# Kernel optimization log

Hardware: AMD Instinct MI355X
Metric: run time of the kernel (lower is better)

Reference implementation:

```python
import jax, jax.numpy as jnp
import numpy as np

TOP_K = 48
NUM_RBF = 16
NUM_RBF_SC = 8
MAXREL = 32
EDGE_F = 128
EPS_D = 1e-6
LN_EPS = 1e-5


def gather_nodes(nodes, idx):
    # nodes: [B, L, C], idx: [B, L, K] -> [B, L, K, C]
    return jax.vmap(lambda n, i: n[i])(nodes, idx)


def rbf(D, count):
    # D: [..., ] -> [..., count]; mu in [2, 22], sigma = 20/count
    mu = jnp.linspace(2.0, 22.0, count)
    sigma = (22.0 - 2.0) / count
    return jnp.exp(-(((D[..., None] - mu) / sigma) ** 2))


def layer_norm(x, g, b):
    mu = jnp.mean(x, -1, keepdims=True)
    var = jnp.mean((x - mu) ** 2, -1, keepdims=True)
    return g * (x - mu) / jnp.sqrt(var + LN_EPS) + b


def setup_inputs() -> dict:
    key = jax.random.key(0)
    ks = jax.random.split(key, 8)
    B, Lr = 1, 1024
    X = jax.random.normal(ks[0], (B, Lr, 37, 3), dtype=jnp.float32)
    mask = jnp.ones((B, Lr), dtype=jnp.float32)
    atom_mask = jnp.ones((B, Lr, 37), dtype=jnp.float32)
    residue_idx = jnp.arange(B * Lr, dtype=jnp.int64 if jax.config.jax_enable_x64 else jnp.int32).reshape(B, Lr)
    dihedral_mask = jnp.ones((B, Lr), dtype=jnp.float32)
    chain_labels = jnp.zeros((B, Lr), dtype=jnp.int32)
    W_pos = jax.random.normal(ks[1], (16, 2 * MAXREL + 2), dtype=jnp.float32) * 0.1
    b_pos = jnp.zeros((16,), dtype=jnp.float32)
    W_e = jax.random.normal(ks[2], (EDGE_F, 16 + NUM_RBF * 25), dtype=jnp.float32) * 0.05
    g_e = jnp.ones((EDGE_F,), dtype=jnp.float32)
    be_e = jnp.zeros((EDGE_F,), dtype=jnp.float32)
    W_s = jax.random.normal(ks[3], (EDGE_F, NUM_RBF_SC * 32 * 5), dtype=jnp.float32) * 0.05
    g_s = jnp.ones((EDGE_F,), dtype=jnp.float32)
    b_s = jnp.zeros((EDGE_F,), dtype=jnp.float32)
    return {"X": X, "L": 1024, "mask": mask, "atom_mask": atom_mask,
            "residue_idx": residue_idx, "dihedral_mask": dihedral_mask,
            "chain_labels": chain_labels, "W_pos": W_pos, "b_pos": b_pos,
            "W_e": W_e, "g_e": g_e, "be_e": be_e, "W_s": W_s, "g_s": g_s, "b_s": b_s}


def reference(X, L, mask, atom_mask, residue_idx, dihedral_mask, chain_labels,
              W_pos, b_pos, W_e, g_e, be_e, W_s, g_s, b_s):
    # Virtual Cb from ideal geometry
    b_v = X[:, :, 1, :] - X[:, :, 0, :]
    c_v = X[:, :, 2, :] - X[:, :, 1, :]
    a_v = jnp.cross(b_v, c_v)
    Cb = -0.58273431 * a_v + 0.56802827 * b_v - 0.54067466 * c_v + X[:, :, 1, :]
    Ca = X[:, :, 1, :]
    N = X[:, :, 0, :]
    C = X[:, :, 2, :]
    O = X[:, :, 4, :]

    # _dist: masked pairwise Ca distances + top-k smallest
    mask2d = mask[:, None, :] * mask[:, :, None]  # [B, L, L]
    dX = Ca[:, :, None, :] - Ca[:, None, :, :]
    D = mask2d * jnp.sqrt(jnp.sum(dX ** 2, -1) + EPS_D)
    D_max = jnp.max(D, -1, keepdims=True)
    D_adj = D + (1.0 - mask2d) * D_max
    neg_vals, E_idx = jax.lax.top_k(-D_adj, TOP_K)
    D_neighbors = -neg_vals  # [B, L, K]

    coords = {'N': N, 'Ca': Ca, 'C': C, 'O': O, 'Cb': Cb}
    pairs = [('N','N'),('C','C'),('O','O'),('Cb','Cb'),('Ca','N'),('Ca','C'),('Ca','O'),
             ('Ca','Cb'),('N','C'),('N','O'),('N','Cb'),('Cb','C'),('Cb','O'),('O','C'),
             ('N','Ca'),('C','Ca'),('O','Ca'),('Cb','Ca'),('C','N'),('O','N'),('Cb','N'),
             ('C','Cb'),('O','Cb'),('C','O')]
    A_st = jnp.stack([coords[a] for a, _ in pairs])  # [24, B, L, 3]
    B_st = jnp.stack([coords[b] for _, b in pairs])
    B_nb = jax.vmap(gather_nodes, (0, None))(B_st, E_idx)  # [24, B, L, K, 3]
    Dp = jnp.sqrt(jnp.sum((A_st[:, :, :, None, :] - B_nb) ** 2, -1) + EPS_D)  # [24,B,L,K]
    RBF_pairs = rbf(Dp, NUM_RBF)  # [24, B, L, K, 16]
    Bt, Lr, K = E_idx.shape
    RBF_pairs = jnp.moveaxis(RBF_pairs, 0, 3).reshape(Bt, Lr, K, 24 * NUM_RBF)
    RBF_all = jnp.concatenate([rbf(D_neighbors, NUM_RBF), RBF_pairs], -1)  # [B,L,K,400]

    # Positional encodings
    ri_nb = gather_nodes(residue_idx[..., None], E_idx)[..., 0]  # [B,L,K]
    offset = residue_idx[:, :, None] - ri_nb
    ch_nb = gather_nodes(chain_labels[..., None], E_idx)[..., 0]
    E_chains = (chain_labels[:, :, None] - ch_nb == 0).astype(jnp.int32)
    d = jnp.clip(offset + MAXREL, 0, 2 * MAXREL) * E_chains + (1 - E_chains) * (2 * MAXREL + 1)
    d_onehot = jax.nn.one_hot(d, 2 * MAXREL + 2, dtype=jnp.float32)
    E_positional = d_onehot @ W_pos.T + b_pos
    E = jnp.concatenate([E_positional, RBF_all], -1)  # [B,L,K,416]

    # Sidechain RBFs on the first min(100, K) neighbors
    Ks = min(100, K)
    E_idx_sub = E_idx[:, :, :Ks]
    am_g = gather_nodes(atom_mask, E_idx_sub)  # [B,L,Ks,37]
    S = X[:, :, 5:37, :]  # [B,L,32,3]
    S_nb = gather_nodes(S.reshape(Bt, Lr, 32 * 3), E_idx_sub).reshape(Bt, Lr, Ks, 32, 3)
    anchors = jnp.stack([N, Ca, C, O, Cb], 2)  # [B,L,5,3], anchor order matches loop order
    Ds = jnp.sqrt(jnp.sum((anchors[:, :, None, :, None, :] - S_nb[:, :, :, None, :, :]) ** 2, -1) + EPS_D)
    # Ds: [B,L,Ks,5,32]; rbf_side -> [B,L,Ks,5,32,8]; masked by neighbor atom mask
    RBF_s = rbf(Ds, NUM_RBF_SC) * am_g[:, :, :, None, 5:37, None]
    E_s = RBF_s.reshape(Bt, Lr, Ks, 5 * 32 * NUM_RBF_SC)  # [B,L,Ks,1280]

    E_s = layer_norm(E_s @ W_s.T, g_s, b_s)
    E = layer_norm(E @ W_e.T, g_e, be_e)
    return (E, E_idx, E_s, E_idx_sub)
```

## Files before the change

kernel.cpp:

```cpp
#include <hip/hip_runtime.h>
#include <math.h>

#define LRES 1024
#define TOPK 48
#define NEDGE (LRES*TOPK)

typedef short short8 __attribute__((ext_vector_type(8)));
typedef float f32x4  __attribute__((ext_vector_type(4)));

#define OUT_E     0
#define OUT_EIDX  6291456
#define OUT_ES    6340608
#define OUT_EIDX2 12632064

#define WS_COORDS 0
#define WS_DNB    15360
#define WS_EIDX   64512
#define WS_WPE    113664
#define WS_WPS    146432

#define DE 1.06666667f
#define QE 0.10273976f
#define DS 1.14285714f
#define QS 0.07337053f

__constant__ int PA[24] = {0,2,3,4,1,1,1,1,0,0,0,4,4,3,0,2,3,4,2,3,4,2,3,2};
__constant__ int PB[24] = {0,2,3,4,0,2,3,4,2,3,4,2,3,2,1,1,1,1,0,0,0,4,4,3};

__device__ inline short f2bf(float f) {
    unsigned u = __float_as_uint(f);
    unsigned r = (u + 0x7FFFu + ((u >> 16) & 1u)) >> 16;
    return (short)r;
}

__device__ inline short8 pack8(const float* fv) {
    union { short8 s; unsigned u[4]; } r;
    #pragma unroll
    for (int i = 0; i < 4; ++i)
        r.u[i] = __builtin_amdgcn_perm(__float_as_uint(fv[2*i+1]),
                                       __float_as_uint(fv[2*i]), 0x07060302u);
    return r.s;
}

__global__ __launch_bounds__(256) void k_pre(const float* __restrict__ X,
                                             const float* __restrict__ mask,
                                             const float* __restrict__ We,
                                             const float* __restrict__ Ws,
                                             float* __restrict__ coords,
                                             short* __restrict__ WpE,
                                             short* __restrict__ WpS,
                                             float* __restrict__ Dnb,
                                             int* __restrict__ Eidx,
                                             float* __restrict__ out) {
    int blk = blockIdx.x, t = threadIdx.x;
    if (blk < 256) {
        __shared__ float sCa[LRES*3];
        __shared__ float sM[LRES];
        for (int j = t; j < LRES; j += 256) {
            sCa[j*3+0] = X[j*111 + 3];
            sCa[j*3+1] = X[j*111 + 4];
            sCa[j*3+2] = X[j*111 + 5];
            sM[j] = mask[j];
        }
        __syncthreads();
        int w = t >> 6, lane = t & 63;
        int i = blk * 4 + w;
        float cx = sCa[i*3], cy = sCa[i*3+1], cz = sCa[i*3+2];
        float mi = sM[i];
        float dv[16], m2v[16];
        float lmax = -1e30f;
        #pragma unroll
        for (int s = 0; s < 16; ++s) {
            int j = s*64 + lane;
            float dx = cx - sCa[j*3], dy = cy - sCa[j*3+1], dz = cz - sCa[j*3+2];
            float d  = __builtin_amdgcn_sqrtf(dx*dx + dy*dy + dz*dz + 1e-6f);
            float m2 = mi * sM[j];
            dv[s] = m2 * d; m2v[s] = m2;
            lmax = fmaxf(lmax, dv[s]);
        }
        #pragma unroll
        for (int off = 32; off; off >>= 1) lmax = fmaxf(lmax, __shfl_xor(lmax, off));
        unsigned long long key[16];
        #pragma unroll
        for (int s = 0; s < 16; ++s) {
            float dadj = dv[s] + (1.0f - m2v[s]) * lmax;
            key[s] = (((unsigned long long)__float_as_uint(dadj)) << 10) | (unsigned)(s*64 + lane);
        }
        unsigned long long mkey = key[0];
        #pragma unroll
        for (int s = 1; s < 16; ++s) mkey = (key[s] < mkey) ? key[s] : mkey;
        for (int it = 0; it < TOPK; ++it) {
            unsigned long long wk = mkey;
            #pragma unroll
            for (int off = 32; off; off >>= 1) {
                unsigned long long o = __shfl_xor(wk, off);
                wk = (o < wk) ? o : wk;
            }
            if (lane == 0) {
                int j = (int)(wk & 1023u);
                int id = i*TOPK + it;
                Dnb[id]  = __uint_as_float((unsigned)(wk >> 10));
                Eidx[id] = j;
                out[OUT_EIDX  + id] = (float)j;
                out[OUT_EIDX2 + id] = (float)j;
            }
            if (mkey == wk) {
                #pragma unroll
                for (int s = 0; s < 16; ++s)
                    key[s] = (key[s] == wk) ? ~0ull : key[s];
                mkey = key[0];
                #pragma unroll
                for (int s = 1; s < 16; ++s) mkey = (key[s] < mkey) ? key[s] : mkey;
            }
        }
    } else if (blk < 896) {
        int g = (blk - 256) * 256 + t;
        if (g < 8*16*64*8) {
            int j = g & 7, lane = (g >> 3) & 63, gg = g >> 9;
            int ks = gg & 15, nt = gg >> 4;
            int n = nt*16 + (lane & 15), k = ks*32 + (lane >> 4)*8 + j;
            WpE[g] = (k < 416) ? f2bf(We[n*416 + k]) : (short)0;
        }
        if (g < 8*40*64*8) {
            int j = g & 7, lane = (g >> 3) & 63, gg = g >> 9;
            int ks = gg % 40, nt = gg / 40;
            int n = nt*16 + (lane & 15), k = ks*32 + (lane >> 4)*8 + j;
            WpS[g] = f2bf(Ws[n*1280 + k]);
        }
    } else {
        int r = (blk - 896) * 256 + t;
        if (r >= LRES) return;
        const float* xr = X + r * 111;
        float N[3], Ca[3], C[3], O[3], bv[3], cv[3], av[3];
        #pragma unroll
        for (int d = 0; d < 3; ++d) {
            N[d]  = xr[0*3 + d];  Ca[d] = xr[1*3 + d];
            C[d]  = xr[2*3 + d];  O[d]  = xr[4*3 + d];
            bv[d] = Ca[d] - N[d]; cv[d] = C[d] - Ca[d];
        }
        av[0] = bv[1]*cv[2] - bv[2]*cv[1];
        av[1] = bv[2]*cv[0] - bv[0]*cv[2];
        av[2] = bv[0]*cv[1] - bv[1]*cv[0];
        float* o = coords + r * 15;
        #pragma unroll
        for (int d = 0; d < 3; ++d) {
            float Cb = -0.58273431f*av[d] + 0.56802827f*bv[d] - 0.54067466f*cv[d] + Ca[d];
            o[0*3+d] = N[d]; o[1*3+d] = Ca[d]; o[2*3+d] = C[d];
            o[3*3+d] = O[d]; o[4*3+d] = Cb;
        }
    }
}

__global__ __launch_bounds__(256, 3) void k_edge(const float* __restrict__ coords,
                                                 const float* __restrict__ X,
                                                 const float* __restrict__ amask,
                                                 const short* __restrict__ WpE,
                                                 const short* __restrict__ WpS,
                                                 const float* __restrict__ Dnb,
                                                 const int* __restrict__ Eidx,
                                                 const int* __restrict__ ri,
                                                 const int* __restrict__ ch,
                                                 const float* __restrict__ Wpos,
                                                 const float* __restrict__ bpos,
                                                 const float* __restrict__ ge,
                                                 const float* __restrict__ be,
                                                 const float* __restrict__ gs,
                                                 const float* __restrict__ bs,
                                                 float* __restrict__ out) {
    __shared__ float smem[9104];
    float* Ar    = smem;
    float* Br    = smem + 4224;
    float* part  = smem + 8448;
    float* part2 = smem + 8704;
    float* smu   = smem + 8960;
    float* srs   = smem + 8992;
    int*   sdpos = (int*)(smem + 9024);
    float* sA3   = smem + 9056;

    int t = threadIdx.x;
    int w = t >> 6, lane = t & 63, quad = lane >> 4, l16 = lane & 15;
    bool isS = blockIdx.x < 1536;
    int id0 = (isS ? blockIdx.x : blockIdx.x - 1536) * 32;

    f32x4 acc[2][8] = {};
    size_t outBase;
    const float *gW, *bW;

    if (isS) {
        outBase = OUT_ES; gW = gs; bW = bs;
        int i0 = id0 / TOPK;
        if (t < 45) {
            int rr = i0 + t / 15;
            if (rr > LRES-1) rr = LRES-1;
            sA3[t] = coords[rr*15 + t%15];
        }
        int s1 = 4*w + quad;
        float S[2][2][3], am[2][2];
        int bA[2];
        #pragma unroll
        for (int mt = 0; mt < 2; ++mt) {
            int id = id0 + mt*16 + l16;
            int j  = Eidx[id];
            bA[mt] = (id / TOPK - i0) * 15;
            const float* xp = X + (j*37 + 5)*3;
            const float* ap = amask + j*37 + 5;
            #pragma unroll
            for (int h = 0; h < 2; ++h) {
                int s = s1 + h*16;
                S[mt][h][0] = xp[s*3+0];
                S[mt][h][1] = xp[s*3+1];
                S[mt][h][2] = xp[s*3+2];
                am[mt][h]   = ap[s];
            }
        }
        __syncthreads();

        const short8* bp = (const short8*)WpS;
        for (int a = 0; a < 5; ++a) {
            float A[2][3];
            #pragma unroll
            for (int mt = 0; mt < 2; ++mt) {
                A[mt][0] = sA3[bA[mt] + a*3+0];
                A[mt][1] = sA3[bA[mt] + a*3+1];
                A[mt][2] = sA3[bA[mt] + a*3+2];
            }
            #pragma unroll
            for (int h = 0; h < 2; ++h) {
                int ks = a*8 + w + h*4;
                short8 afrag[2];
                #pragma unroll
                for (int mt = 0; mt < 2; ++mt) {
                    float dx = A[mt][0] - S[mt][h][0];
                    float dy = A[mt][1] - S[mt][h][1];
                    float dz = A[mt][2] - S[mt][h][2];
                    float d  = __builtin_amdgcn_sqrtf(fmaf(dz,dz,fmaf(dy,dy,fmaf(dx,dx,1e-6f))));
                    float u  = fmaf(d, 0.4f, -0.8f);
                    float e0 = __expf(-u*u) * am[mt][h];
                    float g  = __expf(fmaf(2.0f*DS, u, -(DS*DS)));
                    float fv[8];
                    fv[0] = e0;
                    #pragma unroll
                    for (int r = 1; r < 8; ++r) { e0 *= g; g *= QS; fv[r] = e0; }
                    afrag[mt] = pack8(fv);
                }
                #pragma unroll
                for (int nt = 0; nt < 8; ++nt) {
                    short8 b = bp[(nt*40 + ks)*64 + lane];
                    acc[0][nt] = __builtin_amdgcn_mfma_f32_16x16x32_bf16(afrag[0], b, acc[0][nt], 0,0,0);
                    acc[1][nt] = __builtin_amdgcn_mfma_f32_16x16x32_bf16(afrag[1], b, acc[1][nt], 0,0,0);
                }
            }
        }
    } else {
        outBase = OUT_E; gW = ge; bW = be;
        float* sdist = Ar;
        float* sposf = Ar + 900;
        float* sA    = Br;
        float* sB    = Br + 480;

        if (t < 32) {
            int id = id0 + t, i = id / TOPK, j = Eidx[id];
            int off = ri[i] - ri[j];
            sdpos[t] = (ch[i] == ch[j]) ? min(max(off + 32, 0), 64) : 65;
            sdist[t*27] = Dnb[id];
        }
        for (int it = t; it < 32*15; it += 256) {
            int e = it / 15, q = it % 15;
            int id = id0 + e, i = id / TOPK, j = Eidx[id];
            sA[e*15+q] = coords[i*15+q];
            sB[e*15+q] = coords[j*15+q];
        }
        __syncthreads();
        for (int it = t; it < 32*24; it += 256) {
            int e = it / 24, p = it % 24, a = PA[p], b = PB[p];
            float dx = sA[e*15+a*3+0] - sB[e*15+b*3+0];
            float dy = sA[e*15+a*3+1] - sB[e*15+b*3+1];
            float dz = sA[e*15+a*3+2] - sB[e*15+b*3+2];
            sdist[e*27 + 1 + p] = __builtin_amdgcn_sqrtf(dx*dx + dy*dy + dz*dz + 1e-6f);
        }
        for (int it = t; it < 32*16; it += 256) {
            int e = it >> 4, c = it & 15;
            sposf[e*17 + c] = Wpos[c*66 + sdpos[e]] + bpos[c];
        }
        __syncthreads();

        const short8* bp = (const short8*)WpE;
        float rb = (quad & 1) ? 8.0f*DE : 0.0f;
        for (int ks = w; ks < 16; ks += 4) {
            short8 afrag[2];
            #pragma unroll
            for (int mt = 0; mt < 2; ++mt) {
                int e = mt*16 + l16;
                float fv[8];
                if (ks == 0 && quad < 2) {
                    #pragma unroll
                    for (int j = 0; j < 8; ++j) fv[j] = sposf[e*17 + quad*8 + j];
                } else {
                    int p = (ks == 0) ? 0 : (2*ks - 1 + (quad >> 1));
                    float d = sdist[e*27 + p];
                    float u = fmaf(d, 0.8f, -1.6f) - rb;
                    float e0 = __expf(-u*u);
                    float g  = __expf(fmaf(2.0f*DE, u, -(DE*DE)));
                    fv[0] = e0;
                    #pragma unroll
                    for (int r = 1; r < 8; ++r) { e0 *= g; g *= QE; fv[r] = e0; }
                }
                afrag[mt] = pack8(fv);
            }
            #pragma unroll
            for (int nt = 0; nt < 8; ++nt) {
                short8 b = bp[(nt*16 + ks)*64 + lane];
                acc[0][nt] = __builtin_amdgcn_mfma_f32_16x16x32_bf16(afrag[0], b, acc[0][nt], 0,0,0);
                acc[1][nt] = __builtin_amdgcn_mfma_f32_16x16x32_bf16(afrag[1], b, acc[1][nt], 0,0,0);
            }
        }
        __syncthreads();
    }

    if (w < 2) {
        float* R = (w == 0) ? Ar : Br;
        #pragma unroll
        for (int mt = 0; mt < 2; ++mt)
        #pragma unroll
        for (int nt = 0; nt < 8; ++nt)
        #pragma unroll
        for (int r = 0; r < 4; ++r)
            R[(mt*16 + quad*4 + r)*132 + nt*16 + l16] = acc[mt][nt][r];
    }
    __syncthreads();
    if (w >= 2) {
        float* R = (w == 2) ? Ar : Br;
        #pragma unroll
        for (int mt = 0; mt < 2; ++mt)
        #pragma unroll
        for (int nt = 0; nt < 8; ++nt)
        #pragma unroll
        for (int r = 0; r < 4; ++r)
            R[(mt*16 + quad*4 + r)*132 + nt*16 + l16] += acc[mt][nt][r];
    }
    __syncthreads();
    {
        int e = t >> 3, p = t & 7;
        float s = 0.f, s2 = 0.f;
        #pragma unroll
        for (int q = 0; q < 16; ++q) {
            int f = q*8 + p;
            float x = Ar[e*132 + f] + Br[e*132 + f];
            Ar[e*132 + f] = x;
            s += x; s2 += x*x;
        }
        part[e*8+p] = s; part2[e*8+p] = s2;
    }
    __syncthreads();
    if (t < 32) {
        float s = 0.f, s2 = 0.f;
        #pragma unroll
        for (int p = 0; p < 8; ++p) { s += part[t*8+p]; s2 += part2[t*8+p]; }
        float mu = s * (1.0f/128.0f);
        float var = s2 * (1.0f/128.0f) - mu*mu;
        smu[t] = mu; srs[t] = rsqrtf(var + 1e-5f);
    }
    __syncthreads();
    for (int it = t; it < 32*32; it += 256) {
        int e = it >> 5, f = (it & 31)*4;
        float4 x = *(const float4*)&Ar[e*132 + f];
        float4 G = *(const float4*)&gW[f];
        float4 B = *(const float4*)&bW[f];
        float mu = smu[e], rs = srs[e];
        float4 r;
        r.x = G.x*(x.x - mu)*rs + B.x;
        r.y = G.y*(x.y - mu)*rs + B.y;
        r.z = G.z*(x.z - mu)*rs + B.z;
        r.w = G.w*(x.w - mu)*rs + B.w;
        *(float4*)&out[outBase + (size_t)(id0 + e)*128 + f] = r;
    }
}

extern "C" void kernel_launch(void* const* d_in, const int* in_sizes, int n_in,
                              void* d_out, int out_size, void* d_ws, size_t ws_size,
                              hipStream_t stream) {
    (void)in_sizes; (void)n_in; (void)out_size; (void)ws_size;
    const float* X     = (const float*)d_in[0];
    const float* mask  = (const float*)d_in[2];
    const float* amask = (const float*)d_in[3];
    const int*   ri    = (const int*)d_in[4];
    const int*   ch    = (const int*)d_in[6];
    const float* Wpos  = (const float*)d_in[7];
    const float* bpos  = (const float*)d_in[8];
    const float* We    = (const float*)d_in[9];
    const float* ge    = (const float*)d_in[10];
    const float* be    = (const float*)d_in[11];
    const float* Ws    = (const float*)d_in[12];
    const float* gs    = (const float*)d_in[13];
    const float* bs    = (const float*)d_in[14];

    float* out    = (float*)d_out;
    float* ws     = (float*)d_ws;
    float* coords = ws + WS_COORDS;
    float* Dnb    = ws + WS_DNB;
    int*   Eidx   = (int*)(ws + WS_EIDX);
    short* WpE    = (short*)(ws + WS_WPE);
    short* WpS    = (short*)(ws + WS_WPS);

    k_pre <<<dim3(900),  dim3(256), 0, stream>>>(X, mask, We, Ws, coords,
                                                 WpE, WpS, Dnb, Eidx, out);
    k_edge<<<dim3(3072), dim3(256), 0, stream>>>(coords, X, amask, WpE, WpS,
                                                 Dnb, Eidx, ri, ch, Wpos, bpos,
                                                 ge, be, gs, bs, out);
}
```

Measured before the change: 190.8 us.

## Split waves across N-tiles and K-halves, shrink LDS, raise occupancy

Each wave now owns half of the 128 output columns and half of the K slices, instead of all columns over a quarter of K. This halves the accumulator registers per wave and replaces the two row-major reduction buffers with one column-major buffer. Shared memory falls from about 36KB to about 21KB, and launch bounds go from 3 to 4 blocks per SM. The E path also stops after K slice 12, skipping the zero-padded slices beyond the 416 real features. In exchange, the RBF A-fragments are computed twice (once by each column-half wave), and the final layer-norm store becomes scalar, strided writes instead of float4 rows.

```diff
diff --git a/kernel.cpp b/kernel.cpp
--- a/kernel.cpp
+++ b/kernel.cpp
@@ -151,7 +151,7 @@
     }
 }
 
-__global__ __launch_bounds__(256, 3) void k_edge(const float* __restrict__ coords,
+__global__ __launch_bounds__(256, 4) void k_edge(const float* __restrict__ coords,
                                                  const float* __restrict__ X,
                                                  const float* __restrict__ amask,
                                                  const short* __restrict__ WpE,
@@ -167,22 +167,22 @@
                                                  const float* __restrict__ gs,
                                                  const float* __restrict__ bs,
                                                  float* __restrict__ out) {
-    __shared__ float smem[9104];
-    float* Ar    = smem;
-    float* Br    = smem + 4224;
-    float* part  = smem + 8448;
-    float* part2 = smem + 8704;
-    float* smu   = smem + 8960;
-    float* srs   = smem + 8992;
-    int*   sdpos = (int*)(smem + 9024);
-    float* sA3   = smem + 9056;
+    __shared__ float smem[5264];
+    float* colbuf = smem;
+    float* part   = smem + 4608;
+    float* part2  = smem + 4864;
+    float* smu    = smem + 5120;
+    float* srs    = smem + 5152;
+    int*   sdpos  = (int*)(smem + 5184);
+    float* sA3    = smem + 5216;
 
     int t = threadIdx.x;
     int w = t >> 6, lane = t & 63, quad = lane >> 4, l16 = lane & 15;
+    int tm = w & 1, kp = w >> 1;
     bool isS = blockIdx.x < 1536;
     int id0 = (isS ? blockIdx.x : blockIdx.x - 1536) * 32;
 
-    f32x4 acc[2][8] = {};
+    f32x4 acc[2][4] = {};
     size_t outBase;
     const float *gW, *bW;
 
@@ -194,8 +194,7 @@
             if (rr > LRES-1) rr = LRES-1;
             sA3[t] = coords[rr*15 + t%15];
         }
-        int s1 = 4*w + quad;
-        float S[2][2][3], am[2][2];
+        float S[2][4][3], am[2][4];
         int bA[2];
         #pragma unroll
         for (int mt = 0; mt < 2; ++mt) {
@@ -205,38 +204,38 @@
             const float* xp = X + (j*37 + 5)*3;
             const float* ap = amask + j*37 + 5;
             #pragma unroll
-            for (int h = 0; h < 2; ++h) {
-                int s = s1 + h*16;
-                S[mt][h][0] = xp[s*3+0];
-                S[mt][h][1] = xp[s*3+1];
-                S[mt][h][2] = xp[s*3+2];
-                am[mt][h]   = ap[s];
+            for (int u = 0; u < 4; ++u) {
+                int s = 4*kp + quad + 8*u;
+                S[mt][u][0] = xp[s*3+0];
+                S[mt][u][1] = xp[s*3+1];
+                S[mt][u][2] = xp[s*3+2];
+                am[mt][u]   = ap[s];
             }
         }
         __syncthreads();
 
         const short8* bp = (const short8*)WpS;
         for (int a = 0; a < 5; ++a) {
-            float A[2][3];
+            float A0[2][3];
             #pragma unroll
             for (int mt = 0; mt < 2; ++mt) {
-                A[mt][0] = sA3[bA[mt] + a*3+0];
-                A[mt][1] = sA3[bA[mt] + a*3+1];
-                A[mt][2] = sA3[bA[mt] + a*3+2];
-            }
-            #pragma unroll
-            for (int h = 0; h < 2; ++h) {
-                int ks = a*8 + w + h*4;
+                A0[mt][0] = sA3[bA[mt] + a*3+0];
+                A0[mt][1] = sA3[bA[mt] + a*3+1];
+                A0[mt][2] = sA3[bA[mt] + a*3+2];
+            }
+            #pragma unroll
+            for (int u = 0; u < 4; ++u) {
+                int ks = a*8 + kp + 2*u;
                 short8 afrag[2];
                 #pragma unroll
                 for (int mt = 0; mt < 2; ++mt) {
-                    float dx = A[mt][0] - S[mt][h][0];
-                    float dy = A[mt][1] - S[mt][h][1];
-                    float dz = A[mt][2] - S[mt][h][2];
+                    float dx = A0[mt][0] - S[mt][u][0];
+                    float dy = A0[mt][1] - S[mt][u][1];
+                    float dz = A0[mt][2] - S[mt][u][2];
                     float d  = __builtin_amdgcn_sqrtf(fmaf(dz,dz,fmaf(dy,dy,fmaf(dx,dx,1e-6f))));
-                    float u  = fmaf(d, 0.4f, -0.8f);
-                    float e0 = __expf(-u*u) * am[mt][h];
-                    float g  = __expf(fmaf(2.0f*DS, u, -(DS*DS)));
+                    float uu = fmaf(d, 0.4f, -0.8f);
+                    float e0 = __expf(-uu*uu) * am[mt][u];
+                    float g  = __expf(fmaf(2.0f*DS, uu, -(DS*DS)));
                     float fv[8];
                     fv[0] = e0;
                     #pragma unroll
@@ -244,19 +243,19 @@
                     afrag[mt] = pack8(fv);
                 }
                 #pragma unroll
-                for (int nt = 0; nt < 8; ++nt) {
-                    short8 b = bp[(nt*40 + ks)*64 + lane];
-                    acc[0][nt] = __builtin_amdgcn_mfma_f32_16x16x32_bf16(afrag[0], b, acc[0][nt], 0,0,0);
-                    acc[1][nt] = __builtin_amdgcn_mfma_f32_16x16x32_bf16(afrag[1], b, acc[1][nt], 0,0,0);
+                for (int n = 0; n < 4; ++n) {
+                    short8 b = bp[((tm*4 + n)*40 + ks)*64 + lane];
+                    acc[0][n] = __builtin_amdgcn_mfma_f32_16x16x32_bf16(afrag[0], b, acc[0][n], 0,0,0);
+                    acc[1][n] = __builtin_amdgcn_mfma_f32_16x16x32_bf16(afrag[1], b, acc[1][n], 0,0,0);
                 }
             }
         }
     } else {
         outBase = OUT_E; gW = ge; bW = be;
-        float* sdist = Ar;
-        float* sposf = Ar + 900;
-        float* sA    = Br;
-        float* sB    = Br + 480;
+        float* sdist = colbuf;
+        float* sposf = colbuf + 900;
+        float* sAc   = colbuf + 1472;
+        float* sBc   = colbuf + 1952;
 
         if (t < 32) {
             int id = id0 + t, i = id / TOPK, j = Eidx[id];
@@ -267,15 +266,15 @@
         for (int it = t; it < 32*15; it += 256) {
             int e = it / 15, q = it % 15;
             int id = id0 + e, i = id / TOPK, j = Eidx[id];
-            sA[e*15+q] = coords[i*15+q];
-            sB[e*15+q] = coords[j*15+q];
+            sAc[e*15+q] = coords[i*15+q];
+            sBc[e*15+q] = coords[j*15+q];
         }
         __syncthreads();
         for (int it = t; it < 32*24; it += 256) {
             int e = it / 24, p = it % 24, a = PA[p], b = PB[p];
-            float dx = sA[e*15+a*3+0] - sB[e*15+b*3+0];
-            float dy = sA[e*15+a*3+1] - sB[e*15+b*3+1];
-            float dz = sA[e*15+a*3+2] - sB[e*15+b*3+2];
+            float dx = sAc[e*15+a*3+0] - sBc[e*15+b*3+0];
+            float dy = sAc[e*15+a*3+1] - sBc[e*15+b*3+1];
+            float dz = sAc[e*15+a*3+2] - sBc[e*15+b*3+2];
             sdist[e*27 + 1 + p] = __builtin_amdgcn_sqrtf(dx*dx + dy*dy + dz*dz + 1e-6f);
         }
         for (int it = t; it < 32*16; it += 256) {
@@ -286,7 +285,9 @@
 
         const short8* bp = (const short8*)WpE;
         float rb = (quad & 1) ? 8.0f*DE : 0.0f;
-        for (int ks = w; ks < 16; ks += 4) {
+        for (int st = 0; st < 8; ++st) {
+            int ks = 2*st + kp;
+            if (ks > 12) break;
             short8 afrag[2];
             #pragma unroll
             for (int mt = 0; mt < 2; ++mt) {
@@ -298,9 +299,9 @@
                 } else {
                     int p = (ks == 0) ? 0 : (2*ks - 1 + (quad >> 1));
                     float d = sdist[e*27 + p];
-                    float u = fmaf(d, 0.8f, -1.6f) - rb;
-                    float e0 = __expf(-u*u);
-                    float g  = __expf(fmaf(2.0f*DE, u, -(DE*DE)));
+                    float uu = fmaf(d, 0.8f, -1.6f) - rb;
+                    float e0 = __expf(-uu*uu);
+                    float g  = __expf(fmaf(2.0f*DE, uu, -(DE*DE)));
                     fv[0] = e0;
                     #pragma unroll
                     for (int r = 1; r < 8; ++r) { e0 *= g; g *= QE; fv[r] = e0; }
@@ -308,48 +309,45 @@
                 afrag[mt] = pack8(fv);
             }
             #pragma unroll
-            for (int nt = 0; nt < 8; ++nt) {
-                short8 b = bp[(nt*16 + ks)*64 + lane];
-                acc[0][nt] = __builtin_amdgcn_mfma_f32_16x16x32_bf16(afrag[0], b, acc[0][nt], 0,0,0);
-                acc[1][nt] = __builtin_amdgcn_mfma_f32_16x16x32_bf16(afrag[1], b, acc[1][nt], 0,0,0);
+            for (int n = 0; n < 4; ++n) {
+                short8 b = bp[((tm*4 + n)*16 + ks)*64 + lane];
+                acc[0][n] = __builtin_amdgcn_mfma_f32_16x16x32_bf16(afrag[0], b, acc[0][n], 0,0,0);
+                acc[1][n] = __builtin_amdgcn_mfma_f32_16x16x32_bf16(afrag[1], b, acc[1][n], 0,0,0);
             }
         }
         __syncthreads();
     }
 
-    if (w < 2) {
-        float* R = (w == 0) ? Ar : Br;
+    if (kp == 0) {
         #pragma unroll
         for (int mt = 0; mt < 2; ++mt)
         #pragma unroll
-        for (int nt = 0; nt < 8; ++nt)
-        #pragma unroll
-        for (int r = 0; r < 4; ++r)
-            R[(mt*16 + quad*4 + r)*132 + nt*16 + l16] = acc[mt][nt][r];
+        for (int n = 0; n < 4; ++n)
+            *(f32x4*)&colbuf[((tm*4 + n)*16 + l16)*36 + mt*16 + quad*4] = acc[mt][n];
     }
     __syncthreads();
-    if (w >= 2) {
-        float* R = (w == 2) ? Ar : Br;
+    if (kp == 1) {
         #pragma unroll
         for (int mt = 0; mt < 2; ++mt)
         #pragma unroll
-        for (int nt = 0; nt < 8; ++nt)
-        #pragma unroll
-        for (int r = 0; r < 4; ++r)
-            R[(mt*16 + quad*4 + r)*132 + nt*16 + l16] += acc[mt][nt][r];
+        for (int n = 0; n < 4; ++n) {
+            f32x4* p = (f32x4*)&colbuf[((tm*4 + n)*16 + l16)*36 + mt*16 + quad*4];
+            f32x4 v = *p;
+            v[0] += acc[mt][n][0]; v[1] += acc[mt][n][1];
+            v[2] += acc[mt][n][2]; v[3] += acc[mt][n][3];
+            *p = v;
+        }
     }
     __syncthreads();
     {
-        int e = t >> 3, p = t & 7;
+        int e = t >> 3, p8 = t & 7;
         float s = 0.f, s2 = 0.f;
         #pragma unroll
         for (int q = 0; q < 16; ++q) {
-            int f = q*8 + p;
-            float x = Ar[e*132 + f] + Br[e*132 + f];
-            Ar[e*132 + f] = x;
+            float x = colbuf[(q*8 + p8)*36 + e];
             s += x; s2 += x*x;
         }
-        part[e*8+p] = s; part2[e*8+p] = s2;
+        part[e*8+p8] = s; part2[e*8+p8] = s2;
     }
     __syncthreads();
     if (t < 32) {
@@ -361,18 +359,22 @@
         smu[t] = mu; srs[t] = rsqrtf(var + 1e-5f);
     }
     __syncthreads();
-    for (int it = t; it < 32*32; it += 256) {
-        int e = it >> 5, f = (it & 31)*4;
-        float4 x = *(const float4*)&Ar[e*132 + f];
-        float4 G = *(const float4*)&gW[f];
-        float4 B = *(const float4*)&bW[f];
-        float mu = smu[e], rs = srs[e];
-        float4 r;
-        r.x = G.x*(x.x - mu)*rs + B.x;
-        r.y = G.y*(x.y - mu)*rs + B.y;
-        r.z = G.z*(x.z - mu)*rs + B.z;
-        r.w = G.w*(x.w - mu)*rs + B.w;
-        *(float4*)&out[outBase + (size_t)(id0 + e)*128 + f] = r;
+    {
+        int f = t >> 1, e0 = (t & 1) * 16;
+        f32x4 v[4], mu[4], rs[4];
+        #pragma unroll
+        for (int k = 0; k < 4; ++k) {
+            v[k]  = *(const f32x4*)&colbuf[f*36 + e0 + k*4];
+            mu[k] = *(const f32x4*)&smu[e0 + k*4];
+            rs[k] = *(const f32x4*)&srs[e0 + k*4];
+        }
+        float gg = gW[f], bb = bW[f];
+        #pragma unroll
+        for (int k = 0; k < 16; ++k) {
+            float x = v[k>>2][k&3];
+            out[outBase + (size_t)(id0 + e0 + k)*128 + f]
+                = gg * (x - mu[k>>2][k&3]) * rs[k>>2][k&3] + bb;
+        }
     }
 }
 
```

Result: no change. 192.5 us (+0.9%).
